# Kernel tuning notes

Hardware: AMD Instinct MI355X
Metric: run time of the kernel (lower is better)

The kernel has to match this reference:

```python
import jax, jax.numpy as jnp
import numpy as np

B, E, C, H = 128, 512, 128, 8
D = E // H
K = 21  # kNN neighbors per electrode (min(21, C))


def setup_inputs() -> dict:
    key = jax.random.key(0)
    ks = jax.random.split(key, 7)
    x = jax.random.normal(ks[0], (B, E, C), dtype=jnp.float32)
    # 1x1 Conv1d with no bias == [E_out, E_in] matmul over the feature dim
    wq = jax.random.normal(ks[1], (E, E), dtype=jnp.float32) * (E ** -0.5)
    wk = jax.random.normal(ks[2], (E, E), dtype=jnp.float32) * (E ** -0.5)
    wv = jax.random.normal(ks[3], (E, E), dtype=jnp.float32) * (E ** -0.5)
    wo = jax.random.normal(ks[4], (E, E), dtype=jnp.float32) * (E ** -0.5)
    dir_vec = jax.random.normal(ks[5], (H, C), dtype=jnp.float32)

    # synthetic electrode positions (stands in for electrode_positions.pt)
    pos = jax.random.normal(ks[6], (C, 3), dtype=jnp.float32)

    # arc_dist: great-circle distance scaled by mean radius
    radii = jnp.linalg.norm(pos, axis=1, keepdims=True)
    posn = pos / radii
    dist = jnp.arccos(jnp.clip(posn @ posn.T, -1.0, 1.0)) * radii.mean()

    # Gaussian spatial bias, row-mean centered
    sigma = jnp.median(jnp.tril(dist, 1))
    attn_bias = -dist ** 2 / (2.0 * sigma ** 2 + 1e-8)
    attn_bias = attn_bias - attn_bias.mean(axis=1, keepdims=True)

    # unit displacement vectors, zeroed on the diagonal: disp[i,j] = unit(pos[j]-pos[i])
    disp = pos[None, :, :] - pos[:, None, :]
    disp = disp / jnp.clip(jnp.linalg.norm(disp, axis=-1, keepdims=True), 1e-8)
    disp = disp.at[jnp.arange(C), jnp.arange(C)].set(0.0)

    # kNN mask: K smallest distances per row (includes self)
    _, knn_idx = jax.lax.top_k(-dist, K)
    knn_mask = jnp.zeros((C, C), dtype=bool).at[jnp.arange(C)[:, None], knn_idx].set(True)

    return {"x": x, "wq": wq, "wk": wk, "wv": wv, "wo": wo,
            "dir_vec": dir_vec, "attn_bias": attn_bias,
            "displacement": disp, "knn_mask": knn_mask}


def reference(x, wq, wk, wv, wo, dir_vec, attn_bias, displacement, knn_mask):
    scale = D ** -0.5
    # q/k/v projections: 1x1 conv (no bias) + SELU, then split heads -> [B,H,D,C]
    q = jax.nn.selu(jnp.einsum('oe,bec->boc', wq, x)).reshape(B, H, D, C)
    k = jax.nn.selu(jnp.einsum('oe,bec->boc', wk, x)).reshape(B, H, D, C)
    v = jax.nn.selu(jnp.einsum('oe,bec->boc', wv, x)).reshape(B, H, D, C)

    # scores[b,h,i,j] = <q[...,i], k[...,j]> * scale + spatial bias
    scores = jnp.einsum('bhdi,bhdj->bhij', q, k) * scale + attn_bias[None, None]

    # per-head antisymmetric directional bias
    dvn = dir_vec / jnp.clip(jnp.linalg.norm(dir_vec, axis=-1, keepdims=True), 1e-12)
    dir_bias = displacement.mean(axis=-1)[None, :, :] * dvn[:, None, :]  # [H,C,C]
    dir_bias = 0.5 * (dir_bias - jnp.swapaxes(dir_bias, -1, -2))
    scores = scores + (dir_bias - dir_bias.mean(axis=-1, keepdims=True))[None]

    # kNN masking + stable softmax
    scores = jnp.where(knn_mask[None, None], scores, -jnp.inf)
    scores = scores - scores.max(axis=-1, keepdims=True)
    p = jax.nn.softmax(scores, axis=-1)

    # aggregate values and merge heads -> [B, E, C]
    attn = jnp.einsum('bhij,bhdj->bhdi', p, v).reshape(B, E, C)
    # output projection (AlphaDropout is identity in eval)
    return jax.nn.selu(jnp.einsum('oe,bec->boc', wo, attn))
```

## Files before the change

### kernel.cpp

```cpp
#include <hip/hip_runtime.h>
#include <math.h>

#define B_ 128
#define E_ 512
#define C_ 128
#define H_ 8
#define D_ 64
#define BEC_ ((size_t)B_ * E_ * C_)

typedef __attribute__((ext_vector_type(8))) __bf16 bf16x8;
typedef __attribute__((ext_vector_type(4))) float f32x4;

__device__ __forceinline__ ushort f2bf(float f) {
    unsigned u = __float_as_uint(f);
    unsigned r = u + 0x7fffu + ((u >> 16) & 1u);
    return (ushort)(r >> 16);
}
__device__ __forceinline__ float bf2f(ushort h) {
    return __uint_as_float(((unsigned)h) << 16);
}
__device__ __forceinline__ void split_bf(float f, ushort& hi, ushort& lo) {
    hi = f2bf(f);
    lo = f2bf(f - bf2f(hi));
}
__device__ __forceinline__ float selu_f(float x) {
    const float alpha = 1.6732632423543772f;
    const float scale = 1.0507009873554805f;
    return x > 0.0f ? scale * x : scale * alpha * expm1f(x);
}
__device__ __forceinline__ void gll16(const void* g, void* l) {
    __builtin_amdgcn_global_load_lds(
        (const __attribute__((address_space(1))) void*)g,
        (__attribute__((address_space(3))) void*)l, 16, 0, 0);
}

__global__ __launch_bounds__(128) void bias_prep_kernel(
    const float* __restrict__ dir_vec, const float* __restrict__ attn_bias,
    const float* __restrict__ disp, const unsigned char* __restrict__ maskb,
    float* __restrict__ combT)
{
    const int i = blockIdx.x, h = blockIdx.y, j = threadIdx.x;
    __shared__ float red[128];
    __shared__ int boolFlag;

    {
        int cnt = 0;
        const int base = j * 16;
#pragma unroll
        for (int t = 0; t < 16; ++t) cnt += (maskb[base + t] != 0);
        red[j] = (float)cnt;
        __syncthreads();
        for (int s = 64; s > 0; s >>= 1) {
            if (j < s) red[j] += red[j + s];
            __syncthreads();
        }
        if (j == 0) boolFlag = (red[0] > 200.0f) ? 1 : 0;
        __syncthreads();
    }

    float dv = dir_vec[h * C_ + j];
    red[j] = dv * dv;
    __syncthreads();
    for (int s = 64; s > 0; s >>= 1) {
        if (j < s) red[j] += red[j + s];
        __syncthreads();
    }
    const float nrm = fmaxf(sqrtf(red[0]), 1e-12f);
    __syncthreads();

    const float dvn_j = dir_vec[h * C_ + j] / nrm;
    const float dvn_i = dir_vec[h * C_ + i] / nrm;
    const float third = 1.0f / 3.0f;
    const float dm_ij = (disp[(i * C_ + j) * 3 + 0] + disp[(i * C_ + j) * 3 + 1] +
                         disp[(i * C_ + j) * 3 + 2]) * third;
    const float dm_ji = (disp[(j * C_ + i) * 3 + 0] + disp[(j * C_ + i) * 3 + 1] +
                         disp[(j * C_ + i) * 3 + 2]) * third;
    const float db = 0.5f * (dm_ij * dvn_j - dm_ji * dvn_i);

    red[j] = db;
    __syncthreads();
    for (int s = 64; s > 0; s >>= 1) {
        if (j < s) red[j] += red[j + s];
        __syncthreads();
    }
    const float rowmean = red[0] * (1.0f / 128.0f);

    const bool mk = boolFlag ? (maskb[i * C_ + j] != 0)
                             : (((const int*)maskb)[i * C_ + j] != 0);
    combT[((size_t)h * C_ + j) * C_ + i] =
        mk ? (attn_bias[i * C_ + j] + db - rowmean) : -INFINITY;
}

__global__ __launch_bounds__(256) void split_kernel(
    const float* __restrict__ w0, const float* __restrict__ w1,
    const float* __restrict__ w2, const float* __restrict__ w3,
    const float* __restrict__ x,
    ushort* __restrict__ wh, ushort* __restrict__ wl,
    ushort* __restrict__ xh, ushort* __restrict__ xl)
{
    __shared__ float ts[64][132];
    const int id = blockIdx.x;
    const int tid = threadIdx.x;

    if (id < 512) {
        const int s = id >> 7;
        const float* __restrict__ w = (s == 0) ? w0 : (s == 1) ? w1
                                    : (s == 2) ? w2 : w3;
        const size_t base = (size_t)s * E_ * E_;
        const size_t i0 = ((size_t)(id & 127) * 256 + tid) * 8;
        const float4 f0 = *(const float4*)&w[i0];
        const float4 f1 = *(const float4*)&w[i0 + 4];
        const float ff[8] = {f0.x, f0.y, f0.z, f0.w, f1.x, f1.y, f1.z, f1.w};
        union { ushort u[8]; uint4 v; } hu, lu;
#pragma unroll
        for (int j = 0; j < 8; ++j) split_bf(ff[j], hu.u[j], lu.u[j]);
        *(uint4*)&wh[base + i0] = hu.v;
        *(uint4*)&wl[base + i0] = lu.v;
        return;
    }

    const int fid = id - 512;
    const int b = fid >> 3, e0 = (fid & 7) * 64;
    const float* __restrict__ xb = x + ((size_t)b * E_ + e0) * C_;
#pragma unroll
    for (int r = 0; r < 8; ++r) {
        const int idx = tid + r * 256;
        const int e = idx >> 5, c4 = idx & 31;
        *(float4*)&ts[e][c4 * 4] = *(const float4*)&xb[(size_t)e * C_ + c4 * 4];
    }
    __syncthreads();
    const int lc = tid >> 3;
    const int l8 = (tid & 7) * 8;
#pragma unroll
    for (int p = 0; p < 4; ++p) {
        const int c = p * 32 + lc;
        union { ushort u[8]; uint4 v; } hu, lu;
#pragma unroll
        for (int j = 0; j < 8; ++j) split_bf(ts[l8 + j][c], hu.u[j], lu.u[j]);
        const size_t rb = ((size_t)b * C_ + c) * E_ + e0 + l8;
        *(uint4*)&xh[rb] = hu.v;
        *(uint4*)&xl[rb] = lu.v;
    }
}

template<int MODE>
__global__ __launch_bounds__(256, 2) void gemm_kernel(
    const ushort* __restrict__ Wh0, const ushort* __restrict__ Wh1,
    const ushort* __restrict__ Wh2, const ushort* __restrict__ Wl0,
    const ushort* __restrict__ Wl1, const ushort* __restrict__ Wl2,
    const ushort* __restrict__ Bh, const ushort* __restrict__ Bl,
    ushort* __restrict__ qh, ushort* __restrict__ ql,
    ushort* __restrict__ kh, ushort* __restrict__ kl,
    ushort* __restrict__ vhp, float* __restrict__ fout)
{
    const int d = blockIdx.x;
    const int xr = d & 7, slot = d >> 3;
    const int G = (MODE == 0) ? 12 : 4;
    const int b = xr + 8 * (slot / G);
    const int u = slot % G;
    const int z = (MODE == 0) ? (u >> 2) : 0;
    const int o0 = (MODE == 0) ? ((u & 3) * 128) : (u * 128);

    const ushort* __restrict__ wh = (z == 0) ? Wh0 : (z == 1) ? Wh1 : Wh2;
    const ushort* __restrict__ wl = (z == 0) ? Wl0 : (z == 1) ? Wl1 : Wl2;
    const bool trans = (MODE == 0) && (z < 2);
    const bool full3 = (MODE == 1) || (z != 2);

    __shared__ ushort sm[4 * 8192];

    const int tid = threadIdx.x;
    const int wid = tid >> 6, lane = tid & 63;
    const int wr64 = (wid >> 1) * 64, wc64 = (wid & 1) * 64;
    const int w4 = wid * 4;
    const int srow = lane >> 3;
    const size_t gco = (size_t)((lane & 7) ^ srow) * 16;

    const char* __restrict__ bhp = (const char*)(Bh + (size_t)b * C_ * E_);
    const char* __restrict__ blp = (const char*)(Bl + (size_t)b * C_ * E_);
    const char* __restrict__ whp = (const char*)wh;
    const char* __restrict__ wlp = (const char*)wl;

    const char* __restrict__ smb = (const char*)sm;
    const int aoffB = trans ? 32768 : 0;
    const int boffB = trans ? 0 : 32768;

    f32x4 acc[4][4];
#pragma unroll
    for (int m = 0; m < 4; ++m)
#pragma unroll
        for (int n = 0; n < 4; ++n) acc[m][n] = (f32x4)0.0f;

    const int l15 = lane & 15;

    for (int k0 = 0; k0 < E_; k0 += 64) {
#pragma unroll
        for (int t = 0; t < 4; ++t) {
            const int inst = w4 + t;
            const int r = inst * 8 + srow;
            const size_t arow = ((size_t)(o0 + r) * E_ + k0) * 2 + gco;
            const size_t brow = ((size_t)r * E_ + k0) * 2 + gco;
            gll16(whp + arow, &sm[inst * 512]);
            if (full3) gll16(wlp + arow, &sm[8192 + inst * 512]);
            gll16(bhp + brow, &sm[16384 + inst * 512]);
            gll16(blp + brow, &sm[24576 + inst * 512]);
        }
        __syncthreads();
#pragma unroll
        for (int kk = 0; kk < 2; ++kk) {
            const int kbyte = kk * 64 + (lane >> 4) * 16;
            bf16x8 ah[4], al[4], bh4[4], bl4[4];
#pragma unroll
            for (int m = 0; m < 4; ++m) {
                const int r = wr64 + m * 16 + l15;
                const int byt = r * 128 + (kbyte ^ ((r & 7) << 4));
                ah[m] = *(const bf16x8*)(smb + aoffB + byt);
                if (full3) al[m] = *(const bf16x8*)(smb + aoffB + 16384 + byt);
            }
#pragma unroll
            for (int n = 0; n < 4; ++n) {
                const int c = wc64 + n * 16 + l15;
                const int byt = c * 128 + (kbyte ^ ((c & 7) << 4));
                bh4[n] = *(const bf16x8*)(smb + boffB + byt);
                bl4[n] = *(const bf16x8*)(smb + boffB + 16384 + byt);
            }
#pragma unroll
            for (int m = 0; m < 4; ++m)
#pragma unroll
                for (int n = 0; n < 4; ++n)
                    acc[m][n] = __builtin_amdgcn_mfma_f32_16x16x32_bf16(
                        ah[m], bh4[n], acc[m][n], 0, 0, 0);
#pragma unroll
            for (int m = 0; m < 4; ++m)
#pragma unroll
                for (int n = 0; n < 4; ++n)
                    acc[m][n] = __builtin_amdgcn_mfma_f32_16x16x32_bf16(
                        ah[m], bl4[n], acc[m][n], 0, 0, 0);
            if (full3) {
#pragma unroll
                for (int m = 0; m < 4; ++m)
#pragma unroll
                    for (int n = 0; n < 4; ++n)
                        acc[m][n] = __builtin_amdgcn_mfma_f32_16x16x32_bf16(
                            al[m], bh4[n], acc[m][n], 0, 0, 0);
            }
        }
        __syncthreads();
    }

    const int lr = (lane >> 4) * 4, lc = lane & 15;
    if (MODE == 1) {
        float* __restrict__ outb = fout + (size_t)b * E_ * C_;
#pragma unroll
        for (int m = 0; m < 4; ++m)
#pragma unroll
            for (int n = 0; n < 4; ++n) {
                float* po = outb + (size_t)(o0 + wr64 + m * 16 + lr) * C_ +
                            wc64 + n * 16 + lc;
                const f32x4 a = acc[m][n];
#pragma unroll
                for (int j = 0; j < 4; ++j) po[(size_t)j * C_] = selu_f(a[j]);
            }
    } else if (z == 2) {
#pragma unroll
        for (int m = 0; m < 4; ++m)
#pragma unroll
            for (int n = 0; n < 4; ++n) {
                const f32x4 a = acc[m][n];
#pragma unroll
                for (int j = 0; j < 4; ++j) {
                    const size_t idx = ((size_t)b * E_ + o0 + wr64 + m * 16 + lr + j) * C_ +
                                       wc64 + n * 16 + lc;
                    vhp[idx] = f2bf(selu_f(a[j]));
                }
            }
    } else {
        ushort* __restrict__ th = z ? kh : qh;
        ushort* __restrict__ tl = z ? kl : ql;
#pragma unroll
        for (int m = 0; m < 4; ++m)
#pragma unroll
            for (int n = 0; n < 4; ++n) {
                const f32x4 a = acc[m][n];
#pragma unroll
                for (int j = 0; j < 4; ++j) {
                    const int c = wr64 + m * 16 + lr + j;
                    const int o = o0 + wc64 + n * 16 + lc;
                    const size_t idx = ((size_t)b * C_ + c) * E_ + o;
                    ushort hi, lo;
                    split_bf(selu_f(a[j]), hi, lo);
                    th[idx] = hi;
                    tl[idx] = lo;
                }
            }
    }
}

__global__ __launch_bounds__(256, 2) void attn_mfma_kernel(
    const ushort* __restrict__ qTh, const ushort* __restrict__ qTl,
    const ushort* __restrict__ kTh, const ushort* __restrict__ kTl,
    const ushort* __restrict__ vh,  const float* __restrict__ combT,
    ushort* __restrict__ aTh, ushort* __restrict__ aTl)
{
    const int dd_ = blockIdx.x;
    const int b = (dd_ & 7) + 8 * ((dd_ >> 3) >> 3);
    const int h = (dd_ >> 3) & 7;
    __shared__ ushort lds[40960];
    ushort* sQh = lds;
    ushort* sQl = lds + 8192;
    ushort* sKh = lds + 16384;
    ushort* sKl = lds + 24576;
    ushort* sV  = lds + 32768;
    ushort* sPh = lds;
    ushort* sPl = lds + 16384;

    const int tid = threadIdx.x, wid = tid >> 6, lane = tid & 63;

    {
        const size_t gq = (size_t)b * C_ * E_ + h * D_;
        const int rsub = lane >> 3, chunk = lane & 7;
#pragma unroll
        for (int t = 0; t < 4; ++t) {
            const int inst = wid * 4 + t;
            const int row = inst * 8 + rsub;
            const size_t goff = (gq + (size_t)row * E_) * 2 +
                                (size_t)(chunk ^ (row & 7)) * 16;
            gll16((const char*)qTh + goff, &sQh[inst * 512]);
            gll16((const char*)qTl + goff, &sQl[inst * 512]);
            gll16((const char*)kTh + goff, &sKh[inst * 512]);
            gll16((const char*)kTl + goff, &sKl[inst * 512]);
        }
        const size_t gv = ((size_t)b * E_ + h * D_) * C_;
        const int vr = lane >> 4, vchunk = lane & 15;
#pragma unroll
        for (int t = 0; t < 4; ++t) {
            const int inst = wid * 4 + t;
            const int row = inst * 4 + vr;
            const size_t goff = (gv + (size_t)row * C_) * 2 +
                                (size_t)(vchunk ^ (row & 7)) * 16;
            gll16((const char*)vh + goff, &sV[inst * 512]);
        }
    }
    __syncthreads();

    const int i0 = wid * 32;
    const int l15 = lane & 15;

    f32x4 acc[2][8];
#pragma unroll
    for (int m = 0; m < 2; ++m)
#pragma unroll
        for (int n = 0; n < 8; ++n) acc[m][n] = (f32x4)0.0f;

#pragma unroll
    for (int kk = 0; kk < 2; ++kk) {
        const int kbyte = kk * 64 + (lane >> 4) * 16;
        bf16x8 qhf[2], qlf[2];
#pragma unroll
        for (int m = 0; m < 2; ++m) {
            const int r = i0 + m * 16 + l15;
            const int byt = r * 128 + (kbyte ^ ((r & 7) << 4));
            qhf[m] = *(const bf16x8*)((const char*)sQh + byt);
            qlf[m] = *(const bf16x8*)((const char*)sQl + byt);
        }
#pragma unroll
        for (int n = 0; n < 8; ++n) {
            const int r = n * 16 + l15;
            const int byt = r * 128 + (kbyte ^ ((r & 7) << 4));
            const bf16x8 khf = *(const bf16x8*)((const char*)sKh + byt);
            const bf16x8 klf = *(const bf16x8*)((const char*)sKl + byt);
#pragma unroll
            for (int m = 0; m < 2; ++m) {
                acc[m][n] = __builtin_amdgcn_mfma_f32_16x16x32_bf16(
                    qhf[m], khf, acc[m][n], 0, 0, 0);
                acc[m][n] = __builtin_amdgcn_mfma_f32_16x16x32_bf16(
                    qhf[m], klf, acc[m][n], 0, 0, 0);
                acc[m][n] = __builtin_amdgcn_mfma_f32_16x16x32_bf16(
                    qlf[m], khf, acc[m][n], 0, 0, 0);
            }
        }
    }

#pragma unroll
    for (int m = 0; m < 2; ++m)
#pragma unroll
        for (int n = 0; n < 8; ++n) {
            const int jcol = n * 16 + l15;
            const float4 cb = *(const float4*)&combT[
                ((size_t)h * C_ + jcol) * C_ + i0 + m * 16 + (lane >> 4) * 4];
            acc[m][n][0] = fmaf(acc[m][n][0], 0.125f, cb.x);
            acc[m][n][1] = fmaf(acc[m][n][1], 0.125f, cb.y);
            acc[m][n][2] = fmaf(acc[m][n][2], 0.125f, cb.z);
            acc[m][n][3] = fmaf(acc[m][n][3], 0.125f, cb.w);
        }

#pragma unroll
    for (int m = 0; m < 2; ++m)
#pragma unroll
        for (int jj = 0; jj < 4; ++jj) {
            float mx = -INFINITY;
#pragma unroll
            for (int n = 0; n < 8; ++n) mx = fmaxf(mx, acc[m][n][jj]);
#pragma unroll
            for (int off = 1; off < 16; off <<= 1)
                mx = fmaxf(mx, __shfl_xor(mx, off));
            float sum = 0.0f;
#pragma unroll
            for (int n = 0; n < 8; ++n) {
                const float e = __expf(acc[m][n][jj] - mx);
                acc[m][n][jj] = e;
                sum += e;
            }
#pragma unroll
            for (int off = 1; off < 16; off <<= 1) sum += __shfl_xor(sum, off);
            const float inv = 1.0f / sum;
#pragma unroll
            for (int n = 0; n < 8; ++n) acc[m][n][jj] *= inv;
        }

    __syncthreads();
#pragma unroll
    for (int m = 0; m < 2; ++m)
#pragma unroll
        for (int n = 0; n < 8; ++n)
#pragma unroll
            for (int jj = 0; jj < 4; ++jj) {
                const int i = i0 + m * 16 + (lane >> 4) * 4 + jj;
                const int col = n * 16 + l15;
                const int byt = i * 256 + ((col * 2) ^ ((i & 7) << 4));
                ushort hi, lo;
                split_bf(acc[m][n][jj], hi, lo);
                *(ushort*)((char*)sPh + byt) = hi;
                *(ushort*)((char*)sPl + byt) = lo;
            }
    __syncthreads();

    f32x4 acc2[2][4];
#pragma unroll
    for (int m = 0; m < 2; ++m)
#pragma unroll
        for (int n = 0; n < 4; ++n) acc2[m][n] = (f32x4)0.0f;

#pragma unroll
    for (int ks = 0; ks < 4; ++ks) {
        const int kbyte = ks * 64 + (lane >> 4) * 16;
        bf16x8 ph[2], pl[2];
#pragma unroll
        for (int m = 0; m < 2; ++m) {
            const int r = i0 + m * 16 + l15;
            const int byt = r * 256 + (kbyte ^ ((r & 7) << 4));
            ph[m] = *(const bf16x8*)((const char*)sPh + byt);
            pl[m] = *(const bf16x8*)((const char*)sPl + byt);
        }
#pragma unroll
        for (int n = 0; n < 4; ++n) {
            const int dcol = n * 16 + l15;
            const int byt = dcol * 256 + (kbyte ^ ((dcol & 7) << 4));
            const bf16x8 vb = *(const bf16x8*)((const char*)sV + byt);
#pragma unroll
            for (int m = 0; m < 2; ++m) {
                acc2[m][n] = __builtin_amdgcn_mfma_f32_16x16x32_bf16(
                    ph[m], vb, acc2[m][n], 0, 0, 0);
                acc2[m][n] = __builtin_amdgcn_mfma_f32_16x16x32_bf16(
                    pl[m], vb, acc2[m][n], 0, 0, 0);
            }
        }
    }

#pragma unroll
    for (int m = 0; m < 2; ++m)
#pragma unroll
        for (int n = 0; n < 4; ++n)
#pragma unroll
            for (int jj = 0; jj < 4; ++jj) {
                const int i = i0 + m * 16 + (lane >> 4) * 4 + jj;
                const int dcol = n * 16 + l15;
                ushort hi, lo;
                split_bf(acc2[m][n][jj], hi, lo);
                const size_t idx = ((size_t)b * C_ + i) * E_ + h * D_ + dcol;
                aTh[idx] = hi;
                aTl[idx] = lo;
            }
}

extern "C" void kernel_launch(void* const* d_in, const int* in_sizes, int n_in,
                              void* d_out, int out_size, void* d_ws, size_t ws_size,
                              hipStream_t stream) {
    const float* x        = (const float*)d_in[0];
    const float* wq       = (const float*)d_in[1];
    const float* wk       = (const float*)d_in[2];
    const float* wv       = (const float*)d_in[3];
    const float* wo       = (const float*)d_in[4];
    const float* dir_vec  = (const float*)d_in[5];
    const float* attn_b   = (const float*)d_in[6];
    const float* disp     = (const float*)d_in[7];
    const unsigned char* knn = (const unsigned char*)d_in[8];
    float* out = (float*)d_out;

    char* ws = (char*)d_ws;
    size_t off = 0;
    ushort* qTh = (ushort*)(ws + off); off += BEC_ * 2;
    ushort* qTl = (ushort*)(ws + off); off += BEC_ * 2;
    ushort* kTh = (ushort*)(ws + off); off += BEC_ * 2;
    ushort* kTl = (ushort*)(ws + off); off += BEC_ * 2;
    ushort* vbuf = (ushort*)(ws + off); off += BEC_ * 2;
    ushort* xTh = (ushort*)(ws + off); off += BEC_ * 2;
    ushort* xTl = (ushort*)(ws + off); off += BEC_ * 2;
    ushort* wh  = (ushort*)(ws + off); off += (size_t)4 * E_ * E_ * 2;
    ushort* wl  = (ushort*)(ws + off); off += (size_t)4 * E_ * E_ * 2;
    float* combT = (float*)(ws + off); off += (size_t)H_ * C_ * C_ * sizeof(float);

    bias_prep_kernel<<<dim3(C_, H_), 128, 0, stream>>>(dir_vec, attn_b, disp,
                                                       knn, combT);
    split_kernel<<<1536, 256, 0, stream>>>(wq, wk, wv, wo, x, wh, wl, xTh, xTl);

    const size_t WSZ = (size_t)E_ * E_;
    gemm_kernel<0><<<1536, 256, 0, stream>>>(
        wh, wh + WSZ, wh + 2 * WSZ, wl, wl + WSZ, wl + 2 * WSZ,
        xTh, xTl, qTh, qTl, kTh, kTl, vbuf, nullptr);
    attn_mfma_kernel<<<1024, 256, 0, stream>>>(
        qTh, qTl, kTh, kTl, vbuf, combT, xTh, xTl);
    gemm_kernel<1><<<512, 256, 0, stream>>>(
        wh + 3 * WSZ, wh + 3 * WSZ, wh + 3 * WSZ,
        wl + 3 * WSZ, wl + 3 * WSZ, wl + 3 * WSZ,
        xTh, xTl, nullptr, nullptr, nullptr, nullptr, nullptr, out);
}
```

Before: 176.0 us.

## Load QKV projection operands directly from global memory, bypassing LDS staging

The QKV projection GEMM is split into its own kernel that reads MFMA operand fragments straight from global memory into registers. This removes the LDS staging and both __syncthreads per k-step, and raises the occupancy hint to 3 blocks per CU. The output-projection GEMM keeps the LDS path in a specialised template. The cost is that reuse of each tile now depends on L1/L2 caching, so global traffic and latency exposure may grow.

```diff
diff --git a/kernel.cpp b/kernel.cpp
--- a/kernel.cpp
+++ b/kernel.cpp
@@ -143,46 +143,50 @@
     }
 }
 
-template<int MODE>
-__global__ __launch_bounds__(256, 2) void gemm_kernel(
+__global__ __launch_bounds__(256, 3) void gemm_direct_kernel(
     const ushort* __restrict__ Wh0, const ushort* __restrict__ Wh1,
     const ushort* __restrict__ Wh2, const ushort* __restrict__ Wl0,
     const ushort* __restrict__ Wl1, const ushort* __restrict__ Wl2,
     const ushort* __restrict__ Bh, const ushort* __restrict__ Bl,
     ushort* __restrict__ qh, ushort* __restrict__ ql,
     ushort* __restrict__ kh, ushort* __restrict__ kl,
-    ushort* __restrict__ vhp, float* __restrict__ fout)
+    ushort* __restrict__ vhp)
 {
     const int d = blockIdx.x;
     const int xr = d & 7, slot = d >> 3;
-    const int G = (MODE == 0) ? 12 : 4;
-    const int b = xr + 8 * (slot / G);
-    const int u = slot % G;
-    const int z = (MODE == 0) ? (u >> 2) : 0;
-    const int o0 = (MODE == 0) ? ((u & 3) * 128) : (u * 128);
+    const int b = xr + 8 * (slot / 12);
+    const int u = slot % 12;
+    const int z = u >> 2;
+    const int o0 = (u & 3) * 128;
 
     const ushort* __restrict__ wh = (z == 0) ? Wh0 : (z == 1) ? Wh1 : Wh2;
     const ushort* __restrict__ wl = (z == 0) ? Wl0 : (z == 1) ? Wl1 : Wl2;
-    const bool trans = (MODE == 0) && (z < 2);
-    const bool full3 = (MODE == 1) || (z != 2);
-
-    __shared__ ushort sm[4 * 8192];
-
-    const int tid = threadIdx.x;
-    const int wid = tid >> 6, lane = tid & 63;
+    const bool trans = (z < 2);
+    const bool full3 = (z != 2);
+
+    const int tid = threadIdx.x, wid = tid >> 6, lane = tid & 63;
     const int wr64 = (wid >> 1) * 64, wc64 = (wid & 1) * 64;
-    const int w4 = wid * 4;
-    const int srow = lane >> 3;
-    const size_t gco = (size_t)((lane & 7) ^ srow) * 16;
-
-    const char* __restrict__ bhp = (const char*)(Bh + (size_t)b * C_ * E_);
-    const char* __restrict__ blp = (const char*)(Bl + (size_t)b * C_ * E_);
-    const char* __restrict__ whp = (const char*)wh;
-    const char* __restrict__ wlp = (const char*)wl;
-
-    const char* __restrict__ smb = (const char*)sm;
-    const int aoffB = trans ? 32768 : 0;
-    const int boffB = trans ? 0 : 32768;
+    const int l15 = lane & 15;
+    const int kch = (lane >> 4) * 16;
+
+    const char* __restrict__ Ahb = trans ? (const char*)Bh : (const char*)wh;
+    const char* __restrict__ Alb = trans ? (const char*)Bl : (const char*)wl;
+    const char* __restrict__ Bhb = trans ? (const char*)wh : (const char*)Bh;
+    const char* __restrict__ Blb = trans ? (const char*)wl : (const char*)Bl;
+
+    unsigned aoff[4], boff[4];
+#pragma unroll
+    for (int m = 0; m < 4; ++m) {
+        const int arow = trans ? (b * C_ + wr64 + m * 16 + l15)
+                               : (o0 + wr64 + m * 16 + l15);
+        aoff[m] = (unsigned)(arow * (E_ * 2)) + kch;
+    }
+#pragma unroll
+    for (int n = 0; n < 4; ++n) {
+        const int brow = trans ? (o0 + wc64 + n * 16 + l15)
+                               : (b * C_ + wc64 + n * 16 + l15);
+        boff[n] = (unsigned)(brow * (E_ * 2)) + kch;
+    }
 
     f32x4 acc[4][4];
 #pragma unroll
@@ -190,77 +194,43 @@
 #pragma unroll
         for (int n = 0; n < 4; ++n) acc[m][n] = (f32x4)0.0f;
 
-    const int l15 = lane & 15;
-
-    for (int k0 = 0; k0 < E_; k0 += 64) {
-#pragma unroll
-        for (int t = 0; t < 4; ++t) {
-            const int inst = w4 + t;
-            const int r = inst * 8 + srow;
-            const size_t arow = ((size_t)(o0 + r) * E_ + k0) * 2 + gco;
-            const size_t brow = ((size_t)r * E_ + k0) * 2 + gco;
-            gll16(whp + arow, &sm[inst * 512]);
-            if (full3) gll16(wlp + arow, &sm[8192 + inst * 512]);
-            gll16(bhp + brow, &sm[16384 + inst * 512]);
-            gll16(blp + brow, &sm[24576 + inst * 512]);
-        }
-        __syncthreads();
-#pragma unroll
-        for (int kk = 0; kk < 2; ++kk) {
-            const int kbyte = kk * 64 + (lane >> 4) * 16;
-            bf16x8 ah[4], al[4], bh4[4], bl4[4];
-#pragma unroll
-            for (int m = 0; m < 4; ++m) {
-                const int r = wr64 + m * 16 + l15;
-                const int byt = r * 128 + (kbyte ^ ((r & 7) << 4));
-                ah[m] = *(const bf16x8*)(smb + aoffB + byt);
-                if (full3) al[m] = *(const bf16x8*)(smb + aoffB + 16384 + byt);
-            }
-#pragma unroll
-            for (int n = 0; n < 4; ++n) {
-                const int c = wc64 + n * 16 + l15;
-                const int byt = c * 128 + (kbyte ^ ((c & 7) << 4));
-                bh4[n] = *(const bf16x8*)(smb + boffB + byt);
-                bl4[n] = *(const bf16x8*)(smb + boffB + 16384 + byt);
-            }
+#pragma unroll 2
+    for (int kb = 0; kb < E_ * 2; kb += 64) {
+        bf16x8 ah[4], al[4], bh4[4], bl4[4];
+#pragma unroll
+        for (int m = 0; m < 4; ++m) {
+            ah[m] = *(const bf16x8*)(Ahb + aoff[m] + kb);
+            if (full3) al[m] = *(const bf16x8*)(Alb + aoff[m] + kb);
+        }
+#pragma unroll
+        for (int n = 0; n < 4; ++n) {
+            bh4[n] = *(const bf16x8*)(Bhb + boff[n] + kb);
+            bl4[n] = *(const bf16x8*)(Blb + boff[n] + kb);
+        }
+#pragma unroll
+        for (int m = 0; m < 4; ++m)
+#pragma unroll
+            for (int n = 0; n < 4; ++n)
+                acc[m][n] = __builtin_amdgcn_mfma_f32_16x16x32_bf16(
+                    ah[m], bh4[n], acc[m][n], 0, 0, 0);
+#pragma unroll
+        for (int m = 0; m < 4; ++m)
+#pragma unroll
+            for (int n = 0; n < 4; ++n)
+                acc[m][n] = __builtin_amdgcn_mfma_f32_16x16x32_bf16(
+                    ah[m], bl4[n], acc[m][n], 0, 0, 0);
+        if (full3) {
 #pragma unroll
             for (int m = 0; m < 4; ++m)
 #pragma unroll
                 for (int n = 0; n < 4; ++n)
                     acc[m][n] = __builtin_amdgcn_mfma_f32_16x16x32_bf16(
-                        ah[m], bh4[n], acc[m][n], 0, 0, 0);
-#pragma unroll
-            for (int m = 0; m < 4; ++m)
-#pragma unroll
-                for (int n = 0; n < 4; ++n)
-                    acc[m][n] = __builtin_amdgcn_mfma_f32_16x16x32_bf16(
-                        ah[m], bl4[n], acc[m][n], 0, 0, 0);
-            if (full3) {
-#pragma unroll
-                for (int m = 0; m < 4; ++m)
-#pragma unroll
-                    for (int n = 0; n < 4; ++n)
-                        acc[m][n] = __builtin_amdgcn_mfma_f32_16x16x32_bf16(
-                            al[m], bh4[n], acc[m][n], 0, 0, 0);
-            }
-        }
-        __syncthreads();
+                        al[m], bh4[n], acc[m][n], 0, 0, 0);
+        }
     }
 
     const int lr = (lane >> 4) * 4, lc = lane & 15;
-    if (MODE == 1) {
-        float* __restrict__ outb = fout + (size_t)b * E_ * C_;
-#pragma unroll
-        for (int m = 0; m < 4; ++m)
-#pragma unroll
-            for (int n = 0; n < 4; ++n) {
-                float* po = outb + (size_t)(o0 + wr64 + m * 16 + lr) * C_ +
-                            wc64 + n * 16 + lc;
-                const f32x4 a = acc[m][n];
-#pragma unroll
-                for (int j = 0; j < 4; ++j) po[(size_t)j * C_] = selu_f(a[j]);
-            }
-    } else if (z == 2) {
+    if (z == 2) {
 #pragma unroll
         for (int m = 0; m < 4; ++m)
 #pragma unroll
@@ -293,6 +263,113 @@
                 }
             }
     }
+}
+
+template<int MODE>
+__global__ __launch_bounds__(256, 2) void gemm_kernel(
+    const ushort* __restrict__ Wh0, const ushort* __restrict__ Wl0,
+    const ushort* __restrict__ Bh, const ushort* __restrict__ Bl,
+    float* __restrict__ fout)
+{
+    const int d = blockIdx.x;
+    const int xr = d & 7, slot = d >> 3;
+    const int G = 4;
+    const int b = xr + 8 * (slot / G);
+    const int u = slot % G;
+    const int o0 = u * 128;
+
+    const ushort* __restrict__ wh = Wh0;
+    const ushort* __restrict__ wl = Wl0;
+
+    __shared__ ushort sm[4 * 8192];
+
+    const int tid = threadIdx.x;
+    const int wid = tid >> 6, lane = tid & 63;
+    const int wr64 = (wid >> 1) * 64, wc64 = (wid & 1) * 64;
+    const int w4 = wid * 4;
+    const int srow = lane >> 3;
+    const size_t gco = (size_t)((lane & 7) ^ srow) * 16;
+
+    const char* __restrict__ bhp = (const char*)(Bh + (size_t)b * C_ * E_);
+    const char* __restrict__ blp = (const char*)(Bl + (size_t)b * C_ * E_);
+    const char* __restrict__ whp = (const char*)wh;
+    const char* __restrict__ wlp = (const char*)wl;
+
+    const char* __restrict__ smb = (const char*)sm;
+
+    f32x4 acc[4][4];
+#pragma unroll
+    for (int m = 0; m < 4; ++m)
+#pragma unroll
+        for (int n = 0; n < 4; ++n) acc[m][n] = (f32x4)0.0f;
+
+    const int l15 = lane & 15;
+
+    for (int k0 = 0; k0 < E_; k0 += 64) {
+#pragma unroll
+        for (int t = 0; t < 4; ++t) {
+            const int inst = w4 + t;
+            const int r = inst * 8 + srow;
+            const size_t arow = ((size_t)(o0 + r) * E_ + k0) * 2 + gco;
+            const size_t brow = ((size_t)r * E_ + k0) * 2 + gco;
+            gll16(whp + arow, &sm[inst * 512]);
+            gll16(wlp + arow, &sm[8192 + inst * 512]);
+            gll16(bhp + brow, &sm[16384 + inst * 512]);
+            gll16(blp + brow, &sm[24576 + inst * 512]);
+        }
+        __syncthreads();
+#pragma unroll
+        for (int kk = 0; kk < 2; ++kk) {
+            const int kbyte = kk * 64 + (lane >> 4) * 16;
+            bf16x8 ah[4], al[4], bh4[4], bl4[4];
+#pragma unroll
+            for (int m = 0; m < 4; ++m) {
+                const int r = wr64 + m * 16 + l15;
+                const int byt = r * 128 + (kbyte ^ ((r & 7) << 4));
+                ah[m] = *(const bf16x8*)(smb + byt);
+                al[m] = *(const bf16x8*)(smb + 16384 + byt);
+            }
+#pragma unroll
+            for (int n = 0; n < 4; ++n) {
+                const int c = wc64 + n * 16 + l15;
+                const int byt = c * 128 + (kbyte ^ ((c & 7) << 4));
+                bh4[n] = *(const bf16x8*)(smb + 32768 + byt);
+                bl4[n] = *(const bf16x8*)(smb + 32768 + 16384 + byt);
+            }
+#pragma unroll
+            for (int m = 0; m < 4; ++m)
+#pragma unroll
+                for (int n = 0; n < 4; ++n)
+                    acc[m][n] = __builtin_amdgcn_mfma_f32_16x16x32_bf16(
+                        ah[m], bh4[n], acc[m][n], 0, 0, 0);
+#pragma unroll
+            for (int m = 0; m < 4; ++m)
+#pragma unroll
+                for (int n = 0; n < 4; ++n)
+                    acc[m][n] = __builtin_amdgcn_mfma_f32_16x16x32_bf16(
+                        ah[m], bl4[n], acc[m][n], 0, 0, 0);
+#pragma unroll
+            for (int m = 0; m < 4; ++m)
+#pragma unroll
+                for (int n = 0; n < 4; ++n)
+                    acc[m][n] = __builtin_amdgcn_mfma_f32_16x16x32_bf16(
+                        al[m], bh4[n], acc[m][n], 0, 0, 0);
+        }
+        __syncthreads();
+    }
+
+    const int lr = (lane >> 4) * 4, lc = lane & 15;
+    float* __restrict__ outb = fout + (size_t)b * E_ * C_;
+#pragma unroll
+    for (int m = 0; m < 4; ++m)
+#pragma unroll
+        for (int n = 0; n < 4; ++n) {
+            float* po = outb + (size_t)(o0 + wr64 + m * 16 + lr) * C_ +
+                        wc64 + n * 16 + lc;
+            const f32x4 a = acc[m][n];
+#pragma unroll
+            for (int j = 0; j < 4; ++j) po[(size_t)j * C_] = selu_f(a[j]);
+        }
 }
 
 __global__ __launch_bounds__(256, 2) void attn_mfma_kernel(
@@ -514,13 +591,11 @@
     split_kernel<<<1536, 256, 0, stream>>>(wq, wk, wv, wo, x, wh, wl, xTh, xTl);
 
     const size_t WSZ = (size_t)E_ * E_;
-    gemm_kernel<0><<<1536, 256, 0, stream>>>(
+    gemm_direct_kernel<<<1536, 256, 0, stream>>>(
         wh, wh + WSZ, wh + 2 * WSZ, wl, wl + WSZ, wl + 2 * WSZ,
-        xTh, xTl, qTh, qTl, kTh, kTl, vbuf, nullptr);
+        xTh, xTl, qTh, qTl, kTh, kTl, vbuf);
     attn_mfma_kernel<<<1024, 256, 0, stream>>>(
         qTh, qTl, kTh, kTl, vbuf, combT, xTh, xTl);
     gemm_kernel<1><<<512, 256, 0, stream>>>(
-        wh + 3 * WSZ, wh + 3 * WSZ, wh + 3 * WSZ,
-        wl + 3 * WSZ, wl + 3 * WSZ, wl + 3 * WSZ,
-        xTh, xTl, nullptr, nullptr, nullptr, nullptr, nullptr, out);
-}
+        wh + 3 * WSZ, wl + 3 * WSZ, xTh, xTl, out);
+}
```

Result: slower. 374.2 us (+112.6%).

## Double-buffer projection GEMM LDS staging with 32-wide K tiles

Applied to the files above, without the earlier changes.

Restructures the projection GEMM main loop to use two LDS buffers with 32-element K slices. The next slice's global-to-LDS loads are issued while MFMAs run on the current one, so there is one barrier per step instead of a load, sync, compute, sync sequence. Each wave now stages a single operand plane (weight hi, weight lo, activation hi or lo) using precomputed offsets and a new XOR swizzle. This trades more, shorter iterations and barriers for overlap of memory latency with compute.

```diff
diff --git a/kernel.cpp b/kernel.cpp
--- a/kernel.cpp
+++ b/kernel.cpp
@@ -166,23 +166,38 @@
     const bool trans = (MODE == 0) && (z < 2);
     const bool full3 = (MODE == 1) || (z != 2);
 
-    __shared__ ushort sm[4 * 8192];
+    __shared__ ushort sm[2 * 16384];
 
     const int tid = threadIdx.x;
     const int wid = tid >> 6, lane = tid & 63;
     const int wr64 = (wid >> 1) * 64, wc64 = (wid & 1) * 64;
-    const int w4 = wid * 4;
-    const int srow = lane >> 3;
-    const size_t gco = (size_t)((lane & 7) ^ srow) * 16;
+    const int l15 = lane & 15;
 
     const char* __restrict__ bhp = (const char*)(Bh + (size_t)b * C_ * E_);
     const char* __restrict__ blp = (const char*)(Bl + (size_t)b * C_ * E_);
-    const char* __restrict__ whp = (const char*)wh;
-    const char* __restrict__ wlp = (const char*)wl;
-
-    const char* __restrict__ smb = (const char*)sm;
-    const int aoffB = trans ? 32768 : 0;
-    const int boffB = trans ? 0 : 32768;
+
+    const char* __restrict__ sptr =
+        (wid == 0) ? (const char*)wh : (wid == 1) ? (const char*)wl
+      : (wid == 2) ? bhp : blp;
+    const int rowbase = (wid < 2) ? o0 : 0;
+    const unsigned chunkSwz = (unsigned)(((lane & 3) ^ ((lane >> 3) & 3)) * 16);
+    unsigned sgo[8];
+#pragma unroll
+    for (int inst = 0; inst < 8; ++inst)
+        sgo[inst] = (unsigned)((rowbase + inst * 16 + (lane >> 2)) * (E_ * 2)) +
+                    chunkSwz;
+    const bool doStage = full3 || (wid != 1);
+
+    const int koff = ((lane >> 4) ^ ((l15 >> 1) & 3)) << 4;
+    const int aPl = trans ? 16384 : 0;
+    const int bPl = trans ? 0 : 16384;
+    int aoffs[4], boffs[4];
+#pragma unroll
+    for (int m = 0; m < 4; ++m)
+        aoffs[m] = aPl + (wr64 + m * 16 + l15) * 64 + koff;
+#pragma unroll
+    for (int n = 0; n < 4; ++n)
+        boffs[n] = bPl + (wc64 + n * 16 + l15) * 64 + koff;
 
     f32x4 acc[4][4];
 #pragma unroll
@@ -190,60 +205,56 @@
 #pragma unroll
         for (int n = 0; n < 4; ++n) acc[m][n] = (f32x4)0.0f;
 
-    const int l15 = lane & 15;
-
-    for (int k0 = 0; k0 < E_; k0 += 64) {
-#pragma unroll
-        for (int t = 0; t < 4; ++t) {
-            const int inst = w4 + t;
-            const int r = inst * 8 + srow;
-            const size_t arow = ((size_t)(o0 + r) * E_ + k0) * 2 + gco;
-            const size_t brow = ((size_t)r * E_ + k0) * 2 + gco;
-            gll16(whp + arow, &sm[inst * 512]);
-            if (full3) gll16(wlp + arow, &sm[8192 + inst * 512]);
-            gll16(bhp + brow, &sm[16384 + inst * 512]);
-            gll16(blp + brow, &sm[24576 + inst * 512]);
-        }
-        __syncthreads();
-#pragma unroll
-        for (int kk = 0; kk < 2; ++kk) {
-            const int kbyte = kk * 64 + (lane >> 4) * 16;
-            bf16x8 ah[4], al[4], bh4[4], bl4[4];
-#pragma unroll
-            for (int m = 0; m < 4; ++m) {
-                const int r = wr64 + m * 16 + l15;
-                const int byt = r * 128 + (kbyte ^ ((r & 7) << 4));
-                ah[m] = *(const bf16x8*)(smb + aoffB + byt);
-                if (full3) al[m] = *(const bf16x8*)(smb + aoffB + 16384 + byt);
-            }
-#pragma unroll
-            for (int n = 0; n < 4; ++n) {
-                const int c = wc64 + n * 16 + l15;
-                const int byt = c * 128 + (kbyte ^ ((c & 7) << 4));
-                bh4[n] = *(const bf16x8*)(smb + boffB + byt);
-                bl4[n] = *(const bf16x8*)(smb + boffB + 16384 + byt);
-            }
+    if (doStage) {
+#pragma unroll
+        for (int inst = 0; inst < 8; ++inst)
+            gll16(sptr + sgo[inst], &sm[wid * 4096 + inst * 512]);
+    }
+    __syncthreads();
+
+    for (int t = 0; t < 16; ++t) {
+        const char* __restrict__ bb = (const char*)sm + (t & 1) * 32768;
+
+        if (t < 15 && doStage) {
+            ushort* nb = sm + ((t + 1) & 1) * 16384;
+            const unsigned kadd = (unsigned)(t + 1) * 64;
+#pragma unroll
+            for (int inst = 0; inst < 8; ++inst)
+                gll16(sptr + sgo[inst] + kadd, &nb[wid * 4096 + inst * 512]);
+        }
+
+        bf16x8 ah[4], al[4], bh4[4], bl4[4];
+#pragma unroll
+        for (int m = 0; m < 4; ++m) {
+            ah[m] = *(const bf16x8*)(bb + aoffs[m]);
+            if (full3) al[m] = *(const bf16x8*)(bb + aoffs[m] + 8192);
+        }
+#pragma unroll
+        for (int n = 0; n < 4; ++n) {
+            bh4[n] = *(const bf16x8*)(bb + boffs[n]);
+            bl4[n] = *(const bf16x8*)(bb + boffs[n] + 8192);
+        }
+#pragma unroll
+        for (int m = 0; m < 4; ++m)
+#pragma unroll
+            for (int n = 0; n < 4; ++n)
+                acc[m][n] = __builtin_amdgcn_mfma_f32_16x16x32_bf16(
+                    ah[m], bh4[n], acc[m][n], 0, 0, 0);
+#pragma unroll
+        for (int m = 0; m < 4; ++m)
+#pragma unroll
+            for (int n = 0; n < 4; ++n)
+                acc[m][n] = __builtin_amdgcn_mfma_f32_16x16x32_bf16(
+                    ah[m], bl4[n], acc[m][n], 0, 0, 0);
+        if (full3) {
 #pragma unroll
             for (int m = 0; m < 4; ++m)
 #pragma unroll
                 for (int n = 0; n < 4; ++n)
                     acc[m][n] = __builtin_amdgcn_mfma_f32_16x16x32_bf16(
-                        ah[m], bh4[n], acc[m][n], 0, 0, 0);
-#pragma unroll
-            for (int m = 0; m < 4; ++m)
-#pragma unroll
-                for (int n = 0; n < 4; ++n)
-                    acc[m][n] = __builtin_amdgcn_mfma_f32_16x16x32_bf16(
-                        ah[m], bl4[n], acc[m][n], 0, 0, 0);
-            if (full3) {
-#pragma unroll
-                for (int m = 0; m < 4; ++m)
-#pragma unroll
-                    for (int n = 0; n < 4; ++n)
-                        acc[m][n] = __builtin_amdgcn_mfma_f32_16x16x32_bf16(
-                            al[m], bh4[n], acc[m][n], 0, 0, 0);
-            }
-        }
+                        al[m], bh4[n], acc[m][n], 0, 0, 0);
+        }
+
         __syncthreads();
     }
 
```

New measurement: 183.9 us. +4.5%, slower.
